# Kernel optimization log

Measured on AMD Instinct MI355X. Metric: run time of the kernel, lower is better.

Reference implementation:

```python
import jax, jax.numpy as jnp
import numpy as np

B, N, K, NCLS = 64, 6000, 100, 21
R, FG_PER = 256, 64
FG_THRESH, BG_HI, BG_LO = 0.5, 0.5, 0.0
VALID_GT = 80


def _iou_one(rois, gt):
    # rois [Nt,4], gt [K,4] -> IoU [Nt,K] with the +1 pixel convention
    wr = rois[:, 2] - rois[:, 0] + 1.0
    hr = rois[:, 3] - rois[:, 1] + 1.0
    wg = gt[:, 2] - gt[:, 0] + 1.0
    hg = gt[:, 3] - gt[:, 1] + 1.0
    area_r = wr * hr
    area_g = wg * hg
    iw = jnp.clip(jnp.minimum(rois[:, None, 2], gt[None, :, 2]) - jnp.maximum(rois[:, None, 0], gt[None, :, 0]) + 1.0, 0.0)
    ih = jnp.clip(jnp.minimum(rois[:, None, 3], gt[None, :, 3]) - jnp.maximum(rois[:, None, 1], gt[None, :, 1]) + 1.0, 0.0)
    inter = iw * ih
    ov = inter / (area_r[:, None] + area_g[None, :] - inter)
    gt_zero = (wg == 1.0) & (hg == 1.0)     # all-zero padded gt rows
    roi_zero = (wr == 1.0) & (hr == 1.0)
    ov = jnp.where(gt_zero[None, :], 0.0, ov)
    ov = jnp.where(roi_zero[:, None], -1.0, ov)
    return ov


def _bbox_transform(ex, gt):
    ew = ex[..., 2] - ex[..., 0] + 1.0
    eh = ex[..., 3] - ex[..., 1] + 1.0
    ecx = ex[..., 0] + 0.5 * ew
    ecy = ex[..., 1] + 0.5 * eh
    gw = gt[..., 2] - gt[..., 0] + 1.0
    gh = gt[..., 3] - gt[..., 1] + 1.0
    gcx = gt[..., 0] + 0.5 * gw
    gcy = gt[..., 1] + 0.5 * gh
    return jnp.stack([(gcx - ecx) / ew, (gcy - ecy) / eh, jnp.log(gw / ew), jnp.log(gh / eh)], axis=-1)


def _sample_one(max_ov, gt_assign, lbls, rois_i, gt_i, key, img_idx):
    # per-image fg/bg sampling with fixed output size R (jit-friendly)
    Nt = max_ov.shape[0]
    kf, kb, kr = jax.random.split(key, 3)
    fg_mask = max_ov >= FG_THRESH
    bg_mask = (max_ov < BG_HI) & (max_ov >= BG_LO)
    fg_count = fg_mask.sum()
    bg_count = bg_mask.sum()
    # random permutation of fg indices; bg indices in original order
    fg_order = jnp.argsort(jnp.where(fg_mask, jax.random.uniform(kf, (Nt,)), 2.0))
    bg_order = jnp.argsort(jnp.where(bg_mask, jnp.arange(Nt, dtype=jnp.float32) / Nt, 2.0))
    j = jnp.arange(R)
    fg_this = jnp.where(bg_count > 0, jnp.minimum(FG_PER, fg_count), jnp.where(fg_count > 0, R, 0))
    rfg = jax.random.uniform(kr, (R,))
    rbg = jax.random.uniform(kb, (R,))
    fg_rep = fg_order[(rfg * jnp.maximum(fg_count, 1)).astype(jnp.int32)]  # with replacement (bg_count==0 branch)
    fg_pick = jnp.where(j < fg_count, fg_order[jnp.minimum(j, Nt - 1)], fg_rep)
    bg_pick = bg_order[(rbg * jnp.maximum(bg_count, 1)).astype(jnp.int32)]  # with replacement, as npr.rand*bg_num
    keep = jnp.where(j < fg_this, fg_pick, bg_pick)
    lab = jnp.where(j < fg_this, lbls[keep], 0.0)
    rois_out = rois_i[keep].at[:, 0].set(img_idx)
    gt_out = gt_i[gt_assign[keep]]
    return lab, rois_out, gt_out


def _forward(all_rois, gt_boxes, bbox_means, bbox_stds, bbox_inside_w):
    Bb, Kk = gt_boxes.shape[0], gt_boxes.shape[1]
    gt_append = jnp.concatenate([jnp.zeros_like(gt_boxes[:, :, :1]), gt_boxes[:, :, :4]], axis=-1)
    rois_all = jnp.concatenate([all_rois, gt_append], axis=1)            # [B, N+K, 5]
    overlaps = jax.vmap(_iou_one)(rois_all[:, :, 1:5], gt_boxes[:, :, :4])  # [B, N+K, K]
    max_ov = overlaps.max(axis=2)
    gt_assign = overlaps.argmax(axis=2)
    labels = jnp.take_along_axis(gt_boxes[:, :, 4], gt_assign, axis=1)   # [B, N+K]
    keys = jax.random.split(jax.random.key(42), Bb)
    img_ids = jnp.arange(Bb, dtype=all_rois.dtype)
    labels_batch, rois_batch, gt_rois_batch = jax.vmap(_sample_one)(max_ov, gt_assign, labels, rois_all, gt_boxes, keys, img_ids)
    targets = _bbox_transform(rois_batch[:, :, 1:5], gt_rois_batch[:, :, :4])
    targets = (targets - bbox_means) / bbox_stds
    fg = labels_batch > 0
    bbox_targets = jnp.where(fg[..., None], targets, 0.0)
    bbox_inside_weights = jnp.where(fg[..., None], bbox_inside_w, 0.0)
    bbox_outside_weights = (bbox_inside_weights > 0).astype(jnp.float32)
    return rois_batch, labels_batch, bbox_targets, bbox_inside_weights, bbox_outside_weights


def setup_inputs():
    key = jax.random.key(0)
    ks = jax.random.split(key, 10)
    rx1 = jax.random.uniform(ks[0], (B, N), minval=0.0, maxval=760.0)
    ry1 = jax.random.uniform(ks[1], (B, N), minval=0.0, maxval=560.0)
    rw = jax.random.uniform(ks[2], (B, N), minval=4.0, maxval=240.0)
    rh = jax.random.uniform(ks[3], (B, N), minval=4.0, maxval=240.0)
    all_rois = jnp.stack([jnp.zeros((B, N)), rx1, ry1, rx1 + rw, ry1 + rh], axis=-1).astype(jnp.float32)
    gx1 = jax.random.uniform(ks[4], (B, K), minval=0.0, maxval=700.0)
    gy1 = jax.random.uniform(ks[5], (B, K), minval=0.0, maxval=500.0)
    gw = jax.random.uniform(ks[6], (B, K), minval=20.0, maxval=200.0)
    gh = jax.random.uniform(ks[7], (B, K), minval=20.0, maxval=200.0)
    cls = jax.random.randint(ks[8], (B, K), 1, NCLS).astype(jnp.float32)
    gt = jnp.stack([gx1, gy1, gx1 + gw, gy1 + gh, cls], axis=-1)
    valid = jnp.arange(K) < VALID_GT
    gt_boxes = jnp.where(valid[None, :, None], gt, 0.0).astype(jnp.float32)
    return {
        'all_rois': all_rois,
        'gt_boxes': gt_boxes,
        'num_boxes': jnp.full((B,), VALID_GT, dtype=jnp.int32),
        'bbox_means': jnp.zeros(4, jnp.float32),
        'bbox_stds': jnp.array([0.1, 0.1, 0.2, 0.2], jnp.float32),
        'bbox_inside_w': jnp.ones(4, jnp.float32),
    }


def reference(all_rois, gt_boxes, num_boxes, bbox_means, bbox_stds, bbox_inside_w):
    # num_boxes is accepted (as in the torch forward signature) but unused, matching the source
    return _forward(all_rois, gt_boxes, bbox_means, bbox_stds, bbox_inside_w)
```

## Files before the change

### kernel.cpp

```cpp
#include <hip/hip_runtime.h>
#include <stdint.h>

#define NB    64
#define NROI  6000
#define KGT   100
#define NT    6100
#define ROUT  256
#define FGPER 64

#define BLOCKA 256
#define ROIS_PER_BLOCK (BLOCKA * 2)
#define NCHA ((NT + ROIS_PER_BLOCK - 1) / ROIS_PER_BLOCK)
#define CHUNK 8

#define BLOCK 512
#define NWAVE (BLOCK / 64)
#define SEG 96
#define SEGW (SEG / NWAVE)
#define CANDMAX 128

#define CLS_FG 2
#define CLS_BG 1
#define CLS_NEG 0

__device__ __forceinline__ uint32_t rotl32(uint32_t v, int s) { return (v << s) | (v >> (32 - s)); }

#define TFR(r) { x0 += x1; x1 = rotl32(x1, r); x1 ^= x0; }
__device__ __forceinline__ void tf2x32(uint32_t k0, uint32_t k1, uint32_t& x0, uint32_t& x1) {
  uint32_t k2 = k0 ^ k1 ^ 0x1BD11BDAu;
  x0 += k0; x1 += k1;
  TFR(13) TFR(15) TFR(26) TFR(6)
  x0 += k1; x1 += k2 + 1u;
  TFR(17) TFR(29) TFR(16) TFR(24)
  x0 += k2; x1 += k0 + 2u;
  TFR(13) TFR(15) TFR(26) TFR(6)
  x0 += k0; x1 += k1 + 3u;
  TFR(17) TFR(29) TFR(16) TFR(24)
  x0 += k1; x1 += k2 + 4u;
  TFR(13) TFR(15) TFR(26) TFR(6)
  x0 += k2; x1 += k0 + 5u;
}

__device__ __forceinline__ uint32_t tf_bits32(uint32_t k0, uint32_t k1, uint32_t idx) {
  uint32_t x0 = 0u, x1 = idx;
  tf2x32(k0, k1, x0, x1);
  return x0 ^ x1;
}

__device__ __forceinline__ float u01f(uint32_t bits) {
  return __uint_as_float((bits >> 9) | 0x3F800000u) - 1.0f;
}

__device__ __forceinline__ float crdiv(float num, float den) {
  bool f0, f1;
  float ds = __builtin_amdgcn_div_scalef(num, den, false, &f0);
  float ns = __builtin_amdgcn_div_scalef(num, den, true,  &f1);
  float r  = __builtin_amdgcn_rcpf(ds);
  float e0 = __builtin_fmaf(-ds, r, 1.0f);
  float r1 = __builtin_fmaf(e0, r, r);
  float m  = ns * r1;
  float e1 = __builtin_fmaf(-ds, m, ns);
  float r2 = __builtin_fmaf(e1, r1, m);
  float e2 = __builtin_fmaf(-ds, r2, ns);
  float fm = __builtin_amdgcn_div_fmasf(e2, r1, r2, f1);
  return __builtin_amdgcn_div_fixupf(fm, den, num);
}

__global__ __launch_bounds__(BLOCKA) void iou_kernel(
    const float* __restrict__ all_rois,
    const float* __restrict__ gt_boxes,
    unsigned short* __restrict__ cls_ws)
{
#pragma clang fp contract(off)
  __shared__ float s_gx1[KGT], s_gy1[KGT], s_gx2[KGT], s_gy2[KGT];
  __shared__ float4 s_cg[KGT + CHUNK];
  __shared__ float s_car[KGT + CHUNK];
  __shared__ short s_ck[KGT];
  __shared__ unsigned long long s_zm[2];
  __shared__ int s_V, s_minz;

  const int b = blockIdx.y;
  const int tid = threadIdx.x;
  const int lane = tid & 63, wv = tid >> 6;

  bool nz = false;
  float gx1v = 0, gy1v = 0, gx2v = 0, gy2v = 0, garv = 0;
  if (tid < KGT) {
    const float* g = gt_boxes + ((size_t)b * KGT + tid) * 5;
    gx1v = g[0]; gy1v = g[1]; gx2v = g[2]; gy2v = g[3];
    s_gx1[tid] = gx1v; s_gy1[tid] = gy1v; s_gx2[tid] = gx2v; s_gy2[tid] = gy2v;
    float wg = __fadd_rn(__fadd_rn(gx2v, -gx1v), 1.0f);
    float hg = __fadd_rn(__fadd_rn(gy2v, -gy1v), 1.0f);
    garv = __fmul_rn(wg, hg);
    nz = !(wg == 1.0f && hg == 1.0f);
  }
  if (wv < 2) {
    unsigned long long bm = __ballot(nz);
    if (lane == 0) s_zm[wv] = bm;
  }
  __syncthreads();
  if (tid == 0) {
    unsigned long long z0 = s_zm[0], z1 = s_zm[1];
    unsigned long long g0 = ~z0;
    unsigned long long g1 = (~z1) & ((1ull << (KGT - 64)) - 1ull);
    int mz = -1;
    if (g0) mz = __ffsll((long long)g0) - 1;
    else if (g1) mz = 64 + __ffsll((long long)g1) - 1;
    s_minz = mz;
    s_V = __popcll(z0) + __popcll(z1);
  }
  if (tid < KGT && nz) {
    unsigned long long lm = (1ull << lane) - 1ull;
    int pos = (wv == 0) ? __popcll(s_zm[0] & lm)
                        : __popcll(s_zm[0]) + __popcll(s_zm[1] & lm);
    s_cg[pos] = make_float4(gx1v, gy1v, gx2v, gy2v);
    s_car[pos] = garv; s_ck[pos] = (short)tid;
  }
  __syncthreads();
  const int V = s_V, minz = s_minz;

  if (tid < CHUNK) { s_cg[V + tid] = make_float4(0.f, 0.f, 0.f, 0.f); s_car[V + tid] = 1.0f; }
  __syncthreads();

  const int base = blockIdx.x * ROIS_PER_BLOCK;
  const int t0 = base + tid, t1 = base + BLOCKA + tid;

  float x1a, y1a, x2a, y2a, x1b, y1b, x2b, y2b;
  {
    int ta = (t0 < NT) ? t0 : 0;
    if (ta < NROI) {
      const float* p = all_rois + ((size_t)b * NROI + ta) * 5;
      x1a = p[1]; y1a = p[2]; x2a = p[3]; y2a = p[4];
    } else {
      int k = ta - NROI;
      x1a = s_gx1[k]; y1a = s_gy1[k]; x2a = s_gx2[k]; y2a = s_gy2[k];
    }
    int tb = (t1 < NT) ? t1 : 0;
    if (tb < NROI) {
      const float* p = all_rois + ((size_t)b * NROI + tb) * 5;
      x1b = p[1]; y1b = p[2]; x2b = p[3]; y2b = p[4];
    } else {
      int k = tb - NROI;
      x1b = s_gx1[k]; y1b = s_gy1[k]; x2b = s_gx2[k]; y2b = s_gy2[k];
    }
  }
  float wra = __fadd_rn(__fadd_rn(x2a, -x1a), 1.0f);
  float hra = __fadd_rn(__fadd_rn(y2a, -y1a), 1.0f);
  float ara = __fmul_rn(wra, hra);
  bool rza = (wra == 1.0f && hra == 1.0f);
  float wrb = __fadd_rn(__fadd_rn(x2b, -x1b), 1.0f);
  float hrb = __fadd_rn(__fadd_rn(y2b, -y1b), 1.0f);
  float arb = __fmul_rn(wrb, hrb);
  bool rzb = (wrb == 1.0f && hrb == 1.0f);

  float besta = -2.0f, bestb = -2.0f;
  int bva = -1, bvb = -1;

  for (int c0 = 0; c0 < V; c0 += CHUNK) {
    float4 g[CHUNK];
    float ca[CHUNK];
#pragma unroll
    for (int i = 0; i < CHUNK; ++i) { g[i] = s_cg[c0 + i]; ca[i] = s_car[c0 + i]; }
#pragma unroll
    for (int i = 0; i < CHUNK; ++i) {
      const int vv = c0 + i;
      const float cx1 = g[i].x, cy1 = g[i].y, cx2 = g[i].z, cy2 = g[i].w, car = ca[i];
      {
        float iw = fmaxf(__fadd_rn(__fadd_rn(fminf(x2a, cx2), -fmaxf(x1a, cx1)), 1.0f), 0.0f);
        float ih = fmaxf(__fadd_rn(__fadd_rn(fminf(y2a, cy2), -fmaxf(y1a, cy1)), 1.0f), 0.0f);
        float inter = __fmul_rn(iw, ih);
        float ov = crdiv(inter, __fadd_rn(__fadd_rn(ara, car), -inter));
        if (vv < V && ov > besta) { besta = ov; bva = vv; }
      }
      {
        float iw = fmaxf(__fadd_rn(__fadd_rn(fminf(x2b, cx2), -fmaxf(x1b, cx1)), 1.0f), 0.0f);
        float ih = fmaxf(__fadd_rn(__fadd_rn(fminf(y2b, cy2), -fmaxf(y1b, cy1)), 1.0f), 0.0f);
        float inter = __fmul_rn(iw, ih);
        float ov = crdiv(inter, __fadd_rn(__fadd_rn(arb, car), -inter));
        if (vv < V && ov > bestb) { bestb = ov; bvb = vv; }
      }
    }
  }

  int bka = (bva >= 0) ? (int)s_ck[bva] : 0;
  int bkb = (bvb >= 0) ? (int)s_ck[bvb] : 0;
  if (rza) { besta = -1.0f; bka = 0; }
  else {
    if (besta < 0.0f) { besta = 0.0f; bka = (minz >= 0 ? minz : 0); }
    else if (besta == 0.0f && minz >= 0 && minz < bka) bka = minz;
  }
  if (rzb) { bestb = -1.0f; bkb = 0; }
  else {
    if (bestb < 0.0f) { bestb = 0.0f; bkb = (minz >= 0 ? minz : 0); }
    else if (bestb == 0.0f && minz >= 0 && minz < bkb) bkb = minz;
  }
  int clsa = (besta >= 0.5f) ? CLS_FG : ((besta >= 0.0f) ? CLS_BG : CLS_NEG);
  int clsb = (bestb >= 0.5f) ? CLS_FG : ((bestb >= 0.0f) ? CLS_BG : CLS_NEG);
  if (t0 < NT) cls_ws[(size_t)b * NT + t0] = (unsigned short)((clsa << 8) | bka);
  if (t1 < NT) cls_ws[(size_t)b * NT + t1] = (unsigned short)((clsb << 8) | bkb);
}

__device__ int nth_non(const unsigned short* cp, int n, int mode) {
  int c = 0;
  for (int t = 0; t < NT; ++t) {
    int cls = cp[t] >> 8;
    bool member = (mode == 0) ? (cls == CLS_FG) : (cls == CLS_BG);
    if (!member) { if (c == n) return t; ++c; }
  }
  return NT - 1;
}

__global__ __launch_bounds__(BLOCK) void sample_kernel(
    const float* __restrict__ all_rois,
    const float* __restrict__ gt_boxes,
    const unsigned short* __restrict__ cls_ws,
    const float* __restrict__ bmeans,
    const float* __restrict__ bstds,
    const float* __restrict__ binw,
    float* __restrict__ out)
{
#pragma clang fp contract(off)
  __shared__ float s_gx1[KGT], s_gy1[KGT], s_gx2[KGT], s_gy2[KGT], s_glb[KGT];
  __shared__ uint64_t s_key[NT];
  __shared__ unsigned short s_bidx[NT];
  __shared__ unsigned short s_ford[NT];
  __shared__ int s_cf[SEG], s_cb[SEG];
  __shared__ int s_pf[SEG + 1], s_pb[SEG + 1];
  __shared__ int s_hist[512];
  __shared__ int s_wtot[NWAVE];
  __shared__ uint64_t s_cand[CANDMAX];
  __shared__ int s_crank[CANDMAX];
  __shared__ int s_candN;

  const int b = blockIdx.x;
  const int tid = threadIdx.x;
  const int lane = tid & 63, wv = tid >> 6;
  const unsigned short* cp = cls_ws + (size_t)b * NT;

  if (tid < KGT) {
    const float* g = gt_boxes + ((size_t)b * KGT + tid) * 5;
    s_gx1[tid] = g[0]; s_gy1[tid] = g[1]; s_gx2[tid] = g[2]; s_gy2[tid] = g[3]; s_glb[tid] = g[4];
  }
  s_hist[tid] = 0;
  if (tid < CANDMAX) s_crank[tid] = 0;
  if (tid == 0) s_candN = 0;

  uint32_t kk0 = 0u, kk1 = (uint32_t)b;
  tf2x32(0u, 42u, kk0, kk1);
  uint32_t kf0 = 0u, kf1 = 0u; tf2x32(kk0, kk1, kf0, kf1);
  uint32_t kb0 = 0u, kb1 = 1u; tf2x32(kk0, kk1, kb0, kb1);
  uint32_t kr0 = 0u, kr1 = 2u; tf2x32(kk0, kk1, kr0, kr1);

  int fgbits = 0, bgbits = 0;
#pragma unroll
  for (int i = 0; i < SEGW; ++i) {
    int s = i * NWAVE + wv;
    int t = s * 64 + lane;
    int cls = (t < NT) ? (cp[t] >> 8) : -1;
    bool fg = (cls == CLS_FG);
    bool bg = (cls == CLS_BG);
    unsigned long long bf = __ballot(fg), bb = __ballot(bg);
    if (lane == 0) { s_cf[s] = __popcll(bf); s_cb[s] = __popcll(bb); }
    fgbits |= fg ? (1 << i) : 0;
    bgbits |= bg ? (1 << i) : 0;
  }
  __syncthreads();

  if (wv < 2) {
    int* src = (wv == 0) ? s_cf : s_cb;
    int* dst = (wv == 0) ? s_pf : s_pb;
    int v0 = src[lane];
    int v1 = (lane < SEG - 64) ? src[64 + lane] : 0;
    int x = v0;
    for (int off = 1; off < 64; off <<= 1) { int n = __shfl_up(x, off); if (lane >= off) x += n; }
    int tot0 = __shfl(x, 63);
    int y = v1;
    for (int off = 1; off < 32; off <<= 1) { int n = __shfl_up(y, off); if (lane >= off) y += n; }
    int tot96 = tot0 + __shfl(y, 31);
    dst[lane] = x - v0;
    if (lane < SEG - 64) dst[64 + lane] = tot0 + (y - v1);
    if (lane == 0) dst[SEG] = tot96;
  }
  __syncthreads();
  const int F = s_pf[SEG], Bc = s_pb[SEG];

#pragma unroll
  for (int i = 0; i < SEGW; ++i) {
    int s = i * NWAVE + wv;
    int t = s * 64 + lane;
    bool fg = (fgbits >> i) & 1, bg = (bgbits >> i) & 1;
    unsigned long long bf = __ballot(fg), bb = __ballot(bg);
    unsigned long long lm = (1ull << lane) - 1ull;
    if (fg) {
      uint32_t ub = tf_bits32(kf0, kf1, (uint32_t)t);
      s_key[s_pf[s] + __popcll(bf & lm)] = (((uint64_t)(ub >> 9)) << 32) | (uint32_t)t;
    }
    if (bg) s_bidx[s_pb[s] + __popcll(bb & lm)] = (unsigned short)t;
  }
  __syncthreads();

  if (Bc > 0) {
    for (int i = tid; i < F; i += BLOCK)
      atomicAdd(&s_hist[(int)(s_key[i] >> 46) & 511], 1);
    __syncthreads();
    int hv = s_hist[wv * 64 + lane];
    int hx = hv;
    for (int off = 1; off < 64; off <<= 1) { int n = __shfl_up(hx, off); if (lane >= off) hx += n; }
    if (lane == 63) s_wtot[wv] = hx;
    __syncthreads();
    int woff = 0;
    for (int w = 0; w < wv; ++w) woff += s_wtot[w];
    s_hist[wv * 64 + lane] = woff + hx - hv;
    __syncthreads();
    for (int i = tid; i < F; i += BLOCK) {
      uint64_t k = s_key[i];
      if (s_hist[(int)(k >> 46) & 511] < FGPER) {
        int pos = atomicAdd(&s_candN, 1);
        if (pos < CANDMAX) s_cand[pos] = k;
      }
    }
    __syncthreads();
    int candN = s_candN;
    if (candN <= CANDMAX) {
      int ci = tid >> 2, ch = tid & 3;
      if (ci < candN) {
        uint64_t kc = s_cand[ci];
        int lo = (F * ch) >> 2, hi = (F * (ch + 1)) >> 2;
        int cnt = 0;
        for (int j = lo; j < hi; ++j) cnt += (s_key[j] < kc) ? 1 : 0;
        atomicAdd(&s_crank[ci], cnt);
      }
      __syncthreads();
      if (tid < candN && tid < CANDMAX) {
        int r = s_crank[tid];
        if (r < FGPER) s_ford[r] = (unsigned short)(s_cand[tid] & 0xFFFFull);
      }
    } else {
      for (int i = tid; i < F; i += BLOCK) {
        uint64_t ki = s_key[i];
        int r = 0;
        for (int j = 0; j < F; ++j) r += (s_key[j] < ki) ? 1 : 0;
        s_ford[r] = (unsigned short)(ki & 0xFFFFull);
      }
    }
  } else {
    for (int i = tid; i < F; i += BLOCK) {
      uint64_t ki = s_key[i];
      int r = 0;
      for (int j = 0; j < F; ++j) r += (s_key[j] < ki) ? 1 : 0;
      s_ford[r] = (unsigned short)(ki & 0xFFFFull);
    }
  }
  __syncthreads();

  if (tid < ROUT) {
    const int j = tid;
    float rfg = u01f(tf_bits32(kr0, kr1, (uint32_t)j));
    float rbg = u01f(tf_bits32(kb0, kb1, (uint32_t)j));

    int fg_this = (Bc > 0) ? (F < FGPER ? F : FGPER) : ((F > 0) ? ROUT : 0);
    int keep; float lab;
    if (j < fg_this) {
      int p;
      if (j < F) { p = j; }
      else {
        p = (int)(__fmul_rn(rfg, (float)(F < 1 ? 1 : F)));
        if (p > NT - 1) p = NT - 1;
        if (p < 0) p = 0;
      }
      keep = (p < F) ? (int)s_ford[p] : nth_non(cp, p - F, 0);
      lab = s_glb[cp[keep] & 0xFF];
    } else {
      int q = (int)(__fmul_rn(rbg, (float)(Bc < 1 ? 1 : Bc)));
      if (q > NT - 1) q = NT - 1;
      if (q < 0) q = 0;
      if (Bc > 0) keep = (q < Bc) ? (int)s_bidx[q] : nth_non(cp, q - Bc, 1);
      else        keep = q;
      lab = 0.0f;
    }

    float ex1, ey1, ex2, ey2;
    if (keep < NROI) {
      const float* p = all_rois + ((size_t)b * NROI + keep) * 5;
      ex1 = p[1]; ey1 = p[2]; ex2 = p[3]; ey2 = p[4];
    } else {
      int k = keep - NROI;
      ex1 = s_gx1[k]; ey1 = s_gy1[k]; ex2 = s_gx2[k]; ey2 = s_gy2[k];
    }
    int ga = cp[keep] & 0xFF;
    float gx1 = s_gx1[ga], gy1 = s_gy1[ga], gx2 = s_gx2[ga], gy2 = s_gy2[ga];

    float ew = ex2 - ex1 + 1.0f, eh = ey2 - ey1 + 1.0f;
    float ecx = ex1 + 0.5f * ew, ecy = ey1 + 0.5f * eh;
    float gw = gx2 - gx1 + 1.0f, gh = gy2 - gy1 + 1.0f;
    float gcx = gx1 + 0.5f * gw, gcy = gy1 + 0.5f * gh;
    float tt[4];
    tt[0] = (gcx - ecx) / ew;
    tt[1] = (gcy - ecy) / eh;
    tt[2] = logf(gw / ew);
    tt[3] = logf(gh / eh);
    bool isfg = (lab > 0.0f);

    size_t roff = (size_t)b * ROUT + j;
    float* po = out + roff * 5;
    po[0] = (float)b; po[1] = ex1; po[2] = ey1; po[3] = ex2; po[4] = ey2;
    out[(size_t)NB * ROUT * 5 + roff] = lab;
    float* pt = out + (size_t)NB * ROUT * 6 + roff * 4;
    float* pi = out + (size_t)NB * ROUT * 10 + roff * 4;
    float* pq = out + (size_t)NB * ROUT * 14 + roff * 4;
    for (int c = 0; c < 4; ++c) {
      float tn = (tt[c] - bmeans[c]) / bstds[c];
      float vi = isfg ? binw[c] : 0.0f;
      pt[c] = isfg ? tn : 0.0f;
      pi[c] = vi;
      pq[c] = (vi > 0.0f) ? 1.0f : 0.0f;
    }
  }
}

extern "C" void kernel_launch(void* const* d_in, const int* in_sizes, int n_in,
                              void* d_out, int out_size, void* d_ws, size_t ws_size,
                              hipStream_t stream) {
  const float* all_rois = (const float*)d_in[0];
  const float* gt_boxes = (const float*)d_in[1];
  const float* bmeans = (const float*)d_in[3];
  const float* bstds  = (const float*)d_in[4];
  const float* binw   = (const float*)d_in[5];
  float* out = (float*)d_out;

  unsigned short* cls_ws = (unsigned short*)d_ws;

  iou_kernel<<<dim3(NCHA, NB), dim3(BLOCKA), 0, stream>>>(all_rois, gt_boxes, cls_ws);
  sample_kernel<<<dim3(NB), dim3(BLOCK), 0, stream>>>(all_rois, gt_boxes, cls_ws,
                                                      bmeans, bstds, binw, out);
}
```

Before: 113.4 us.

## Move fg/bg compaction and fg key generation into the parallel IoU kernel

The IoU kernel now counts fg/bg ROIs per block, computes per-block local offsets, generates the Threefry fg sort keys, and writes compacted per-chunk fg keys and bg indices to workspace. The sample kernel (one block per image) only computes a prefix over the chunk counts and copies the compacted segments into shared memory. This shifts the per-image scan and the RNG work from the serial 64-block sample kernel into the widely parallel IoU grid. In exchange it adds extra global writes and reads, a serial single-thread prefix over chunks, and hard-coded workspace offsets.

```diff
diff --git a/kernel.cpp b/kernel.cpp
--- a/kernel.cpp
+++ b/kernel.cpp
@@ -15,13 +15,12 @@
 
 #define BLOCK 512
 #define NWAVE (BLOCK / 64)
-#define SEG 96
-#define SEGW (SEG / NWAVE)
 #define CANDMAX 128
 
 #define CLS_FG 2
 #define CLS_BG 1
 #define CLS_NEG 0
+
 
 __device__ __forceinline__ uint32_t rotl32(uint32_t v, int s) { return (v << s) | (v >> (32 - s)); }
 
@@ -69,7 +68,10 @@
 __global__ __launch_bounds__(BLOCKA) void iou_kernel(
     const float* __restrict__ all_rois,
     const float* __restrict__ gt_boxes,
-    unsigned short* __restrict__ cls_ws)
+    unsigned short* __restrict__ cls_ws,
+    int2* __restrict__ counts,
+    uint64_t* __restrict__ fgk,
+    unsigned short* __restrict__ bgi)
 {
 #pragma clang fp contract(off)
   __shared__ float s_gx1[KGT], s_gy1[KGT], s_gx2[KGT], s_gy2[KGT];
@@ -78,6 +80,7 @@
   __shared__ short s_ck[KGT];
   __shared__ unsigned long long s_zm[2];
   __shared__ int s_V, s_minz;
+  __shared__ int s_segf[8], s_segb[8];
 
   const int b = blockIdx.y;
   const int tid = threadIdx.x;
@@ -198,6 +201,44 @@
   int clsb = (bestb >= 0.5f) ? CLS_FG : ((bestb >= 0.0f) ? CLS_BG : CLS_NEG);
   if (t0 < NT) cls_ws[(size_t)b * NT + t0] = (unsigned short)((clsa << 8) | bka);
   if (t1 < NT) cls_ws[(size_t)b * NT + t1] = (unsigned short)((clsb << 8) | bkb);
+
+  uint32_t kk0 = 0u, kk1 = (uint32_t)b;
+  tf2x32(0u, 42u, kk0, kk1);
+  uint32_t kf0 = 0u, kf1 = 0u; tf2x32(kk0, kk1, kf0, kf1);
+
+  bool fga = (t0 < NT) && (clsa == CLS_FG);
+  bool bga = (t0 < NT) && (clsa == CLS_BG);
+  bool fgb = (t1 < NT) && (clsb == CLS_FG);
+  bool bgb = (t1 < NT) && (clsb == CLS_BG);
+  unsigned long long mfa = __ballot(fga), mba = __ballot(bga);
+  unsigned long long mfb = __ballot(fgb), mbb = __ballot(bgb);
+  if (lane == 0) {
+    s_segf[wv] = __popcll(mfa);     s_segb[wv] = __popcll(mba);
+    s_segf[4 + wv] = __popcll(mfb); s_segb[4 + wv] = __popcll(mbb);
+  }
+  __syncthreads();
+  if (tid == 0) {
+    int af = 0, ab = 0;
+    for (int s2 = 0; s2 < 8; ++s2) {
+      int cf = s_segf[s2], cb = s_segb[s2];
+      s_segf[s2] = af; s_segb[s2] = ab;
+      af += cf; ab += cb;
+    }
+    counts[(size_t)b * NCHA + blockIdx.x] = make_int2(af, ab);
+  }
+  __syncthreads();
+  unsigned long long lm = (1ull << lane) - 1ull;
+  size_t cbase = ((size_t)b * NCHA + blockIdx.x) * 512;
+  if (fga) {
+    uint32_t ub = tf_bits32(kf0, kf1, (uint32_t)t0);
+    fgk[cbase + s_segf[wv] + __popcll(mfa & lm)] = (((uint64_t)(ub >> 9)) << 32) | (uint32_t)t0;
+  }
+  if (bga) bgi[cbase + s_segb[wv] + __popcll(mba & lm)] = (unsigned short)t0;
+  if (fgb) {
+    uint32_t ub = tf_bits32(kf0, kf1, (uint32_t)t1);
+    fgk[cbase + s_segf[4 + wv] + __popcll(mfb & lm)] = (((uint64_t)(ub >> 9)) << 32) | (uint32_t)t1;
+  }
+  if (bgb) bgi[cbase + s_segb[4 + wv] + __popcll(mbb & lm)] = (unsigned short)t1;
 }
 
 __device__ int nth_non(const unsigned short* cp, int n, int mode) {
@@ -214,6 +255,9 @@
     const float* __restrict__ all_rois,
     const float* __restrict__ gt_boxes,
     const unsigned short* __restrict__ cls_ws,
+    const int2* __restrict__ counts,
+    const uint64_t* __restrict__ fgk,
+    const unsigned short* __restrict__ bgi,
     const float* __restrict__ bmeans,
     const float* __restrict__ bstds,
     const float* __restrict__ binw,
@@ -224,8 +268,7 @@
   __shared__ uint64_t s_key[NT];
   __shared__ unsigned short s_bidx[NT];
   __shared__ unsigned short s_ford[NT];
-  __shared__ int s_cf[SEG], s_cb[SEG];
-  __shared__ int s_pf[SEG + 1], s_pb[SEG + 1];
+  __shared__ int s_foff[NCHA + 1], s_boff[NCHA + 1];
   __shared__ int s_hist[512];
   __shared__ int s_wtot[NWAVE];
   __shared__ uint64_t s_cand[CANDMAX];
@@ -245,57 +288,29 @@
   if (tid < CANDMAX) s_crank[tid] = 0;
   if (tid == 0) s_candN = 0;
 
+  if (tid == 0) {
+    int af = 0, ab = 0;
+    for (int c = 0; c < NCHA; ++c) {
+      int2 cc = counts[(size_t)b * NCHA + c];
+      s_foff[c] = af; s_boff[c] = ab;
+      af += cc.x; ab += cc.y;
+    }
+    s_foff[NCHA] = af; s_boff[NCHA] = ab;
+  }
+
   uint32_t kk0 = 0u, kk1 = (uint32_t)b;
   tf2x32(0u, 42u, kk0, kk1);
-  uint32_t kf0 = 0u, kf1 = 0u; tf2x32(kk0, kk1, kf0, kf1);
   uint32_t kb0 = 0u, kb1 = 1u; tf2x32(kk0, kk1, kb0, kb1);
   uint32_t kr0 = 0u, kr1 = 2u; tf2x32(kk0, kk1, kr0, kr1);
-
-  int fgbits = 0, bgbits = 0;
-#pragma unroll
-  for (int i = 0; i < SEGW; ++i) {
-    int s = i * NWAVE + wv;
-    int t = s * 64 + lane;
-    int cls = (t < NT) ? (cp[t] >> 8) : -1;
-    bool fg = (cls == CLS_FG);
-    bool bg = (cls == CLS_BG);
-    unsigned long long bf = __ballot(fg), bb = __ballot(bg);
-    if (lane == 0) { s_cf[s] = __popcll(bf); s_cb[s] = __popcll(bb); }
-    fgbits |= fg ? (1 << i) : 0;
-    bgbits |= bg ? (1 << i) : 0;
-  }
-  __syncthreads();
-
-  if (wv < 2) {
-    int* src = (wv == 0) ? s_cf : s_cb;
-    int* dst = (wv == 0) ? s_pf : s_pb;
-    int v0 = src[lane];
-    int v1 = (lane < SEG - 64) ? src[64 + lane] : 0;
-    int x = v0;
-    for (int off = 1; off < 64; off <<= 1) { int n = __shfl_up(x, off); if (lane >= off) x += n; }
-    int tot0 = __shfl(x, 63);
-    int y = v1;
-    for (int off = 1; off < 32; off <<= 1) { int n = __shfl_up(y, off); if (lane >= off) y += n; }
-    int tot96 = tot0 + __shfl(y, 31);
-    dst[lane] = x - v0;
-    if (lane < SEG - 64) dst[64 + lane] = tot0 + (y - v1);
-    if (lane == 0) dst[SEG] = tot96;
-  }
-  __syncthreads();
-  const int F = s_pf[SEG], Bc = s_pb[SEG];
-
-#pragma unroll
-  for (int i = 0; i < SEGW; ++i) {
-    int s = i * NWAVE + wv;
-    int t = s * 64 + lane;
-    bool fg = (fgbits >> i) & 1, bg = (bgbits >> i) & 1;
-    unsigned long long bf = __ballot(fg), bb = __ballot(bg);
-    unsigned long long lm = (1ull << lane) - 1ull;
-    if (fg) {
-      uint32_t ub = tf_bits32(kf0, kf1, (uint32_t)t);
-      s_key[s_pf[s] + __popcll(bf & lm)] = (((uint64_t)(ub >> 9)) << 32) | (uint32_t)t;
-    }
-    if (bg) s_bidx[s_pb[s] + __popcll(bb & lm)] = (unsigned short)t;
+  __syncthreads();
+  const int F = s_foff[NCHA], Bc = s_boff[NCHA];
+
+  for (int c = wv; c < NCHA; c += NWAVE) {
+    size_t cbase = ((size_t)b * NCHA + c) * 512;
+    int fo = s_foff[c], nf = s_foff[c + 1] - fo;
+    int bo = s_boff[c], nb = s_boff[c + 1] - bo;
+    for (int i = lane; i < nf; i += 64) s_key[fo + i] = fgk[cbase + i];
+    for (int i = lane; i < nb; i += 64) s_bidx[bo + i] = bgi[cbase + i];
   }
   __syncthreads();
 
@@ -428,9 +443,15 @@
   const float* binw   = (const float*)d_in[5];
   float* out = (float*)d_out;
 
-  unsigned short* cls_ws = (unsigned short*)d_ws;
-
-  iou_kernel<<<dim3(NCHA, NB), dim3(BLOCKA), 0, stream>>>(all_rois, gt_boxes, cls_ws);
+  char* ws = (char*)d_ws;
+  unsigned short* cls_ws = (unsigned short*)ws;
+  int2* counts = (int2*)(ws + 780800);
+  uint64_t* fgk = (uint64_t*)(ws + 786944);
+  unsigned short* bgi = (unsigned short*)(ws + 3932672);
+
+  iou_kernel<<<dim3(NCHA, NB), dim3(BLOCKA), 0, stream>>>(all_rois, gt_boxes, cls_ws,
+                                                          counts, fgk, bgi);
   sample_kernel<<<dim3(NB), dim3(BLOCK), 0, stream>>>(all_rois, gt_boxes, cls_ws,
+                                                      counts, fgk, bgi,
                                                       bmeans, bstds, binw, out);
 }
```

Result: no change. 111.7 us (-1.5%).
